# Performance work log

Measured on AMD Instinct MI355X. Metric: run time of the kernel, lower is better.

Reference implementation:

```python
import jax, jax.numpy as jnp
import numpy as np

BATCH = 32
LATENT = 128
NODE_DIM = 8
MAX_NODES = 512
H_NODE = 128   # node_generator hidden
H_EDGE = 64    # edge_generator hidden


def setup_inputs() -> dict:
    key = jax.random.key(0)
    ks = jax.random.split(key, 9)
    s = 0.02
    return {
        "z":   jax.random.normal(ks[0], (BATCH, LATENT), dtype=jnp.float32),
        "W1":  jax.random.normal(ks[1], (LATENT, H_NODE), dtype=jnp.float32) * s,
        "b1":  jnp.zeros((H_NODE,), dtype=jnp.float32),
        "W2":  jax.random.normal(ks[2], (H_NODE, MAX_NODES * NODE_DIM), dtype=jnp.float32) * s,
        "b2":  jnp.zeros((MAX_NODES * NODE_DIM,), dtype=jnp.float32),
        "E1":  jax.random.normal(ks[3], (2 * NODE_DIM, H_EDGE), dtype=jnp.float32) * s,
        "eb1": jnp.zeros((H_EDGE,), dtype=jnp.float32),
        "E2":  jax.random.normal(ks[4], (H_EDGE, 1), dtype=jnp.float32) * s,
        "eb2": jnp.zeros((1,), dtype=jnp.float32),
    }


def reference(z, W1, b1, W2, b2, E1, eb1, E2, eb2):
    B = z.shape[0]
    # node generator: Linear -> ReLU -> Linear, view to [B, N, node_dim]
    h = jax.nn.relu(z @ W1 + b1)
    nodes = (h @ W2 + b2).reshape(B, MAX_NODES, NODE_DIM)

    # all unordered pairs i < j (static indices)
    iu, ju = np.triu_indices(MAX_NODES, k=1)  # [P]
    pair = jnp.concatenate([nodes[:, iu, :], nodes[:, ju, :]], axis=-1)  # [B, P, 2d]

    # edge generator: Linear -> ReLU -> Linear -> Sigmoid
    he = jax.nn.relu(jnp.einsum("bpd,dh->bph", pair, E1) + eb1)
    p = jax.nn.sigmoid(jnp.einsum("bph,ho->bpo", he, E2) + eb2)[..., 0]  # [B, P]

    adj = jnp.zeros((B, MAX_NODES, MAX_NODES), dtype=p.dtype)
    adj = adj.at[:, iu, ju].set(p).at[:, ju, iu].set(p)
    return nodes, adj
```

## Files before the change

### kernel.cpp

```cpp
#include <hip/hip_runtime.h>

#define BATCH 32
#define LATENT 128
#define NODE_DIM 8
#define MAX_NODES 512
#define H_NODE 128
#define H_EDGE 64

typedef _Float16 h2 __attribute__((ext_vector_type(2)));

static __device__ __forceinline__ h2 u32_to_h2(unsigned int x) {
    union { unsigned int u; h2 h; } c; c.u = x; return c.h;
}
static __device__ __forceinline__ unsigned int h2_to_u32(h2 x) {
    union { unsigned int u; h2 h; } c; c.h = x; return c.u;
}

#if __has_builtin(__builtin_amdgcn_fdot2)
#define FDOT2(a, b, c) __builtin_amdgcn_fdot2((a), (b), (c), false)
#else
#define FDOT2(a, b, c) ((c) + (float)(a).x * (float)(b).x + (float)(a).y * (float)(b).y)
#endif

#define UPKH_DWORDS (BATCH * 32 * MAX_NODES)
#define VH_DWORDS   (BATCH * MAX_NODES * 32)

__global__ __launch_bounds__(128) void h_gen(
    const float* __restrict__ z, const float* __restrict__ W1,
    const float* __restrict__ b1, float* __restrict__ Hws)
{
    const int b = blockIdx.x, tid = threadIdx.x;
    __shared__ float sz[LATENT];
    sz[tid] = z[b * LATENT + tid];
    __syncthreads();
    float acc = b1[tid];
#pragma unroll 8
    for (int k = 0; k < LATENT; ++k)
        acc += sz[k] * W1[k * H_NODE + tid];
    Hws[b * H_NODE + tid] = fmaxf(acc, 0.0f);
}

__global__ __launch_bounds__(256) void gen_nodes_uv(
    const float* __restrict__ Hws, const float* __restrict__ W2,
    const float* __restrict__ b2,  const float* __restrict__ E1,
    const float* __restrict__ eb1, const float* __restrict__ E2,
    float* __restrict__ nodes_out, unsigned int* __restrict__ UPKH,
    unsigned int* __restrict__ VH, unsigned int* __restrict__ E2H)
{
    const int b      = blockIdx.x;
    const int mslice = blockIdx.y;
    const int tid    = threadIdx.x;
    const int i0     = mslice * 32;

    __shared__ float sh[H_NODE];
    __shared__ float sE1[2 * NODE_DIM][H_EDGE];
    __shared__ float sEb1[H_EDGE];
    __shared__ float sN[32][NODE_DIM];

    if (tid < H_NODE) sh[tid] = Hws[b * H_NODE + tid];
    for (int idx = tid; idx < 2 * NODE_DIM * H_EDGE; idx += 256)
        (&sE1[0][0])[idx] = E1[idx];
    if (tid < H_EDGE) sEb1[tid] = eb1[tid];

    if (b == 0 && mslice == 0 && tid < 32) {
        h2 w = { (_Float16)E2[2 * tid], (_Float16)E2[2 * tid + 1] };
        E2H[tid] = h2_to_u32(w);
    }
    __syncthreads();

    const int m = mslice * 256 + tid;
    float acc = b2[m];
#pragma unroll 8
    for (int k = 0; k < H_NODE; ++k)
        acc += sh[k] * W2[(size_t)k * (MAX_NODES * NODE_DIM) + m];
    nodes_out[(size_t)b * (MAX_NODES * NODE_DIM) + m] = acc;
    sN[tid >> 3][tid & 7] = acc;
    __syncthreads();

    {
        const int il = tid & 31;
        const int cg = tid >> 5;
#pragma unroll
        for (int rep = 0; rep < 4; ++rep) {
            const int c2 = rep * 8 + cg;
            const int c  = 2 * c2;
            float ua = sEb1[c], ub = sEb1[c + 1];
#pragma unroll
            for (int d = 0; d < NODE_DIM; ++d) {
                const float nd = sN[il][d];
                ua += nd * sE1[d][c];
                ub += nd * sE1[d][c + 1];
            }
            h2 uu = { (_Float16)ua, (_Float16)ub };
            UPKH[((size_t)b * 32 + c2) * MAX_NODES + i0 + il] = h2_to_u32(uu);
        }
    }
    {
        const int jl = tid >> 3;
        const int cq = tid & 7;
#pragma unroll
        for (int rep = 0; rep < 4; ++rep) {
            const int c2 = rep * 8 + cq;
            const int c  = 2 * c2;
            float va = 0.f, vb = 0.f;
#pragma unroll
            for (int d = 0; d < NODE_DIM; ++d) {
                const float nd = sN[jl][d];
                va += nd * sE1[NODE_DIM + d][c];
                vb += nd * sE1[NODE_DIM + d][c + 1];
            }
            h2 vv = { (_Float16)va, (_Float16)vb };
            VH[((size_t)(b * MAX_NODES + i0 + jl) << 5) + c2] = h2_to_u32(vv);
        }
    }
}

__global__ __launch_bounds__(256, 4) void edge_gen(
    const unsigned int* __restrict__ UPKH, const unsigned int* __restrict__ VH,
    const unsigned int* __restrict__ E2H, const float* __restrict__ eb2,
    float* __restrict__ adj)
{
    const int b = blockIdx.y;
    int t = blockIdx.x, bi = 0;
    while (t >= 16 - 2 * bi) { t -= 16 - 2 * bi; ++bi; }
    const int jt = 2 * bi + t;
    const bool partial = (jt >> 1) == bi;

    const int tid  = threadIdx.x;
    const int lane = tid & 63;
    const int wv   = tid >> 6;
    const int i0 = bi * 64, j0 = jt * 32;
    const int i  = i0 + lane;

    __shared__ unsigned int sV[32 * 32];
    __shared__ float P[32][65];

    {
        const float4* src = (const float4*)(VH + ((size_t)(b * MAX_NODES + j0) << 5));
        ((float4*)sV)[tid] = src[tid];
    }

    unsigned int uA[32];
#pragma unroll
    for (int c2 = 0; c2 < 32; ++c2)
        uA[c2] = UPKH[((size_t)b * 32 + c2) * MAX_NODES + i];

    unsigned int wb[32];
#pragma unroll
    for (int c2 = 0; c2 < 32; ++c2) wb[c2] = E2H[c2];

    const float bias = eb2[0];
    float* adjb = adj + (size_t)b * MAX_NODES * MAX_NODES;
    const h2 zh = { (_Float16)0.f, (_Float16)0.f };
    __syncthreads();

#pragma unroll 1
    for (int jj = 0; jj < 8; ++jj) {
        const int jl = wv * 8 + jj;
        const int j  = j0 + jl;
        const float4* vrow = (const float4*)&sV[jl * 32];

        float a0 = 0.f, a1 = 0.f;
#pragma unroll
        for (int q = 0; q < 8; ++q) {
            union { float4 f4; unsigned int u[4]; } vv;
            vv.f4 = vrow[q];
#pragma unroll
            for (int k = 0; k < 4; ++k) {
                const int c2 = 4 * q + k;
                const h2 v = u32_to_h2(vv.u[k]);
                const h2 w = u32_to_h2(wb[c2]);
                h2 s = u32_to_h2(uA[c2]) + v;
                s = __builtin_elementwise_max(s, zh);
                if (k & 1) a1 = FDOT2(s, w, a1);
                else       a0 = FDOT2(s, w, a0);
            }
        }
        const float x = a0 + a1 + bias;
        const float p = __builtin_amdgcn_rcpf(1.0f + __expf(-x));

        if (!partial) {
            adjb[(size_t)j * MAX_NODES + i] = p;
            P[jl][lane] = p;
        } else {
            if (i < j)       { adjb[(size_t)j * MAX_NODES + i] = p;
                               adjb[(size_t)i * MAX_NODES + j] = p; }
            else if (i == j)   adjb[(size_t)j * MAX_NODES + i] = 0.0f;
        }
    }

    if (!partial) {
        __syncthreads();
        const int r = tid & 63;
        const int q = tid >> 6;
        const size_t rowbase = (size_t)(i0 + r) * MAX_NODES + j0 + q * 8;
        float4 o0, o1;
        o0.x = P[q * 8 + 0][r]; o0.y = P[q * 8 + 1][r];
        o0.z = P[q * 8 + 2][r]; o0.w = P[q * 8 + 3][r];
        o1.x = P[q * 8 + 4][r]; o1.y = P[q * 8 + 5][r];
        o1.z = P[q * 8 + 6][r]; o1.w = P[q * 8 + 7][r];
        *(float4*)&adjb[rowbase]     = o0;
        *(float4*)&adjb[rowbase + 4] = o1;
    }
}

extern "C" void kernel_launch(void* const* d_in, const int* in_sizes, int n_in,
                              void* d_out, int out_size, void* d_ws, size_t ws_size,
                              hipStream_t stream)
{
    const float* z   = (const float*)d_in[0];
    const float* W1  = (const float*)d_in[1];
    const float* b1  = (const float*)d_in[2];
    const float* W2  = (const float*)d_in[3];
    const float* b2  = (const float*)d_in[4];
    const float* E1  = (const float*)d_in[5];
    const float* eb1 = (const float*)d_in[6];
    const float* E2  = (const float*)d_in[7];
    const float* eb2 = (const float*)d_in[8];

    float* nodes_out = (float*)d_out;
    float* adj       = (float*)d_out + BATCH * MAX_NODES * NODE_DIM;

    unsigned int* UPKH = (unsigned int*)d_ws;
    unsigned int* VHp  = UPKH + UPKH_DWORDS;
    unsigned int* E2H  = VHp + VH_DWORDS;
    float*        Hws  = (float*)(E2H + 32);

    h_gen<<<BATCH, 128, 0, stream>>>(z, W1, b1, Hws);

    dim3 g1(BATCH, 16);
    gen_nodes_uv<<<g1, 256, 0, stream>>>(Hws, W2, b2, E1, eb1, E2,
                                         nodes_out, UPKH, VHp, E2H);

    dim3 g2(72, BATCH);
    edge_gen<<<g2, 256, 0, stream>>>(UPKH, VHp, E2H, eb2, adj);
}
```

Before: 46.29 us.

## Halve edge tile width to 16 columns and fully unroll four-column ILP

The edge kernel now covers 64x16 tiles instead of 64x32, so the grid doubles to 144 blocks per batch. Each wave handles four j columns at once with a fully unrolled loop and eight independent accumulators, replacing the serial 8-iteration loop. The aim is more blocks to fill the GPU and more instruction-level parallelism per thread. In exchange, the per-thread UPKH row loads and E2H loads are repeated across twice as many blocks, and register pressure rises.

```diff
diff --git a/kernel.cpp b/kernel.cpp
--- a/kernel.cpp
+++ b/kernel.cpp
@@ -122,22 +122,22 @@
 {
     const int b = blockIdx.y;
     int t = blockIdx.x, bi = 0;
-    while (t >= 16 - 2 * bi) { t -= 16 - 2 * bi; ++bi; }
-    const int jt = 2 * bi + t;
-    const bool partial = (jt >> 1) == bi;
+    while (t >= 32 - 4 * bi) { t -= 32 - 4 * bi; ++bi; }
+    const int jt = 4 * bi + t;
+    const bool partial = (jt >> 2) == bi;
 
     const int tid  = threadIdx.x;
     const int lane = tid & 63;
     const int wv   = tid >> 6;
-    const int i0 = bi * 64, j0 = jt * 32;
+    const int i0 = bi * 64, j0 = jt * 16;
     const int i  = i0 + lane;
 
-    __shared__ unsigned int sV[32 * 32];
-    __shared__ float P[32][65];
-
-    {
-        const float4* src = (const float4*)(VH + ((size_t)(b * MAX_NODES + j0) << 5));
-        ((float4*)sV)[tid] = src[tid];
+    __shared__ unsigned int sV[16 * 32];
+    __shared__ float P[16][65];
+
+    if (tid < 128) {
+        const uint4* src = (const uint4*)(VH + ((size_t)(b * MAX_NODES + j0) << 5));
+        ((uint4*)sV)[tid] = src[tid];
     }
 
     unsigned int uA[32];
@@ -154,31 +154,56 @@
     const h2 zh = { (_Float16)0.f, (_Float16)0.f };
     __syncthreads();
 
-#pragma unroll 1
-    for (int jj = 0; jj < 8; ++jj) {
-        const int jl = wv * 8 + jj;
+    const int jbase = wv * 4;
+    const uint4* vr0 = (const uint4*)&sV[(jbase + 0) * 32];
+    const uint4* vr1 = (const uint4*)&sV[(jbase + 1) * 32];
+    const uint4* vr2 = (const uint4*)&sV[(jbase + 2) * 32];
+    const uint4* vr3 = (const uint4*)&sV[(jbase + 3) * 32];
+
+    float acc0a = 0.f, acc0b = 0.f, acc1a = 0.f, acc1b = 0.f;
+    float acc2a = 0.f, acc2b = 0.f, acc3a = 0.f, acc3b = 0.f;
+
+#pragma unroll
+    for (int q = 0; q < 8; ++q) {
+        union { uint4 u4; unsigned int u[4]; } v0, v1, v2, v3;
+        v0.u4 = vr0[q]; v1.u4 = vr1[q]; v2.u4 = vr2[q]; v3.u4 = vr3[q];
+#pragma unroll
+        for (int k = 0; k < 4; ++k) {
+            const int c2 = 4 * q + k;
+            const h2 u = u32_to_h2(uA[c2]);
+            const h2 w = u32_to_h2(wb[c2]);
+            h2 s0 = u + u32_to_h2(v0.u[k]);
+            h2 s1 = u + u32_to_h2(v1.u[k]);
+            h2 s2 = u + u32_to_h2(v2.u[k]);
+            h2 s3 = u + u32_to_h2(v3.u[k]);
+            s0 = __builtin_elementwise_max(s0, zh);
+            s1 = __builtin_elementwise_max(s1, zh);
+            s2 = __builtin_elementwise_max(s2, zh);
+            s3 = __builtin_elementwise_max(s3, zh);
+            if (k & 1) {
+                acc0b = FDOT2(s0, w, acc0b); acc1b = FDOT2(s1, w, acc1b);
+                acc2b = FDOT2(s2, w, acc2b); acc3b = FDOT2(s3, w, acc3b);
+            } else {
+                acc0a = FDOT2(s0, w, acc0a); acc1a = FDOT2(s1, w, acc1a);
+                acc2a = FDOT2(s2, w, acc2a); acc3a = FDOT2(s3, w, acc3a);
+            }
+        }
+    }
+
+    float px[4];
+    px[0] = acc0a + acc0b + bias;
+    px[1] = acc1a + acc1b + bias;
+    px[2] = acc2a + acc2b + bias;
+    px[3] = acc3a + acc3b + bias;
+#pragma unroll
+    for (int jj = 0; jj < 4; ++jj)
+        px[jj] = __builtin_amdgcn_rcpf(1.0f + __expf(-px[jj]));
+
+#pragma unroll
+    for (int jj = 0; jj < 4; ++jj) {
+        const int jl = jbase + jj;
         const int j  = j0 + jl;
-        const float4* vrow = (const float4*)&sV[jl * 32];
-
-        float a0 = 0.f, a1 = 0.f;
-#pragma unroll
-        for (int q = 0; q < 8; ++q) {
-            union { float4 f4; unsigned int u[4]; } vv;
-            vv.f4 = vrow[q];
-#pragma unroll
-            for (int k = 0; k < 4; ++k) {
-                const int c2 = 4 * q + k;
-                const h2 v = u32_to_h2(vv.u[k]);
-                const h2 w = u32_to_h2(wb[c2]);
-                h2 s = u32_to_h2(uA[c2]) + v;
-                s = __builtin_elementwise_max(s, zh);
-                if (k & 1) a1 = FDOT2(s, w, a1);
-                else       a0 = FDOT2(s, w, a0);
-            }
-        }
-        const float x = a0 + a1 + bias;
-        const float p = __builtin_amdgcn_rcpf(1.0f + __expf(-x));
-
+        const float p = px[jj];
         if (!partial) {
             adjb[(size_t)j * MAX_NODES + i] = p;
             P[jl][lane] = p;
@@ -193,14 +218,10 @@
         __syncthreads();
         const int r = tid & 63;
         const int q = tid >> 6;
-        const size_t rowbase = (size_t)(i0 + r) * MAX_NODES + j0 + q * 8;
-        float4 o0, o1;
-        o0.x = P[q * 8 + 0][r]; o0.y = P[q * 8 + 1][r];
-        o0.z = P[q * 8 + 2][r]; o0.w = P[q * 8 + 3][r];
-        o1.x = P[q * 8 + 4][r]; o1.y = P[q * 8 + 5][r];
-        o1.z = P[q * 8 + 6][r]; o1.w = P[q * 8 + 7][r];
-        *(float4*)&adjb[rowbase]     = o0;
-        *(float4*)&adjb[rowbase + 4] = o1;
+        float4 o;
+        o.x = P[q * 4 + 0][r]; o.y = P[q * 4 + 1][r];
+        o.z = P[q * 4 + 2][r]; o.w = P[q * 4 + 3][r];
+        *(float4*)&adjb[(size_t)(i0 + r) * MAX_NODES + j0 + q * 4] = o;
     }
 }
 
@@ -232,6 +253,6 @@
     gen_nodes_uv<<<g1, 256, 0, stream>>>(Hws, W2, b2, E1, eb1, E2,
                                          nodes_out, UPKH, VHp, E2H);
 
-    dim3 g2(72, BATCH);
+    dim3 g2(144, BATCH);
     edge_gen<<<g2, 256, 0, stream>>>(UPKH, VHp, E2H, eb2, adj);
 }
```

Result: slower. 66.69 us (+44.1%).

## Handle diagonal edge tiles as full 64x64 blocks with LDS-transposed symmetric stores

Applied to the files above, without the earlier changes.

Diagonal tiles used to be two 64x32 partial blocks that wrote scattered strided stores in both orientations. They are now one 64x64 block per diagonal that computes all 64 columns into shared memory, then writes the symmetric tile with coalesced float4 row stores and zeros the diagonal. This cuts the grid from 72 to 64 blocks per batch and removes the uncoalesced scalar writes. In exchange the diagonal blocks compute redundant pairs (j<i) and the larger shared memory footprint may lower occupancy.

```diff
diff --git a/kernel.cpp b/kernel.cpp
--- a/kernel.cpp
+++ b/kernel.cpp
@@ -115,29 +115,58 @@
     }
 }
 
+static __device__ __forceinline__ float edge_dot(
+    const uint4* vrow, const unsigned int (&uA)[32], const unsigned int (&wb)[32])
+{
+    const h2 zh = { (_Float16)0.f, (_Float16)0.f };
+    float a0 = 0.f, a1 = 0.f;
+#pragma unroll
+    for (int q = 0; q < 8; ++q) {
+        union { uint4 u4; unsigned int u[4]; } vv;
+        vv.u4 = vrow[q];
+#pragma unroll
+        for (int k = 0; k < 4; ++k) {
+            const int c2 = 4 * q + k;
+            const h2 v = u32_to_h2(vv.u[k]);
+            const h2 w = u32_to_h2(wb[c2]);
+            h2 s = u32_to_h2(uA[c2]) + v;
+            s = __builtin_elementwise_max(s, zh);
+            if (k & 1) a1 = FDOT2(s, w, a1);
+            else       a0 = FDOT2(s, w, a0);
+        }
+    }
+    return a0 + a1;
+}
+
 __global__ __launch_bounds__(256, 4) void edge_gen(
     const unsigned int* __restrict__ UPKH, const unsigned int* __restrict__ VH,
     const unsigned int* __restrict__ E2H, const float* __restrict__ eb2,
     float* __restrict__ adj)
 {
     const int b = blockIdx.y;
-    int t = blockIdx.x, bi = 0;
-    while (t >= 16 - 2 * bi) { t -= 16 - 2 * bi; ++bi; }
-    const int jt = 2 * bi + t;
-    const bool partial = (jt >> 1) == bi;
-
+    const int x = blockIdx.x;
     const int tid  = threadIdx.x;
     const int lane = tid & 63;
     const int wv   = tid >> 6;
-    const int i0 = bi * 64, j0 = jt * 32;
+
+    __shared__ unsigned int sV[64 * 32];
+    __shared__ float P[64][65];
+
+    int bi, j0, nj;
+    if (x < 8) { bi = x; j0 = bi * 64; nj = 64; }
+    else {
+        int k = x - 8; bi = 0;
+        while (k >= 14 - 2 * bi) { k -= 14 - 2 * bi; ++bi; }
+        j0 = (2 * bi + 2 + k) * 32; nj = 32;
+    }
+    const int i0 = bi * 64;
     const int i  = i0 + lane;
 
-    __shared__ unsigned int sV[32 * 32];
-    __shared__ float P[32][65];
-
     {
-        const float4* src = (const float4*)(VH + ((size_t)(b * MAX_NODES + j0) << 5));
-        ((float4*)sV)[tid] = src[tid];
+        const uint4* src = (const uint4*)(VH + ((size_t)(b * MAX_NODES + j0) << 5));
+        uint4* dst = (uint4*)sV;
+        dst[tid] = src[tid];
+        if (nj == 64) dst[tid + 256] = src[tid + 256];
     }
 
     unsigned int uA[32];
@@ -151,45 +180,18 @@
 
     const float bias = eb2[0];
     float* adjb = adj + (size_t)b * MAX_NODES * MAX_NODES;
-    const h2 zh = { (_Float16)0.f, (_Float16)0.f };
-    __syncthreads();
-
+    __syncthreads();
+
+    if (nj == 32) {
 #pragma unroll 1
-    for (int jj = 0; jj < 8; ++jj) {
-        const int jl = wv * 8 + jj;
-        const int j  = j0 + jl;
-        const float4* vrow = (const float4*)&sV[jl * 32];
-
-        float a0 = 0.f, a1 = 0.f;
-#pragma unroll
-        for (int q = 0; q < 8; ++q) {
-            union { float4 f4; unsigned int u[4]; } vv;
-            vv.f4 = vrow[q];
-#pragma unroll
-            for (int k = 0; k < 4; ++k) {
-                const int c2 = 4 * q + k;
-                const h2 v = u32_to_h2(vv.u[k]);
-                const h2 w = u32_to_h2(wb[c2]);
-                h2 s = u32_to_h2(uA[c2]) + v;
-                s = __builtin_elementwise_max(s, zh);
-                if (k & 1) a1 = FDOT2(s, w, a1);
-                else       a0 = FDOT2(s, w, a0);
-            }
-        }
-        const float x = a0 + a1 + bias;
-        const float p = __builtin_amdgcn_rcpf(1.0f + __expf(-x));
-
-        if (!partial) {
+        for (int jj = 0; jj < 8; ++jj) {
+            const int jl = wv * 8 + jj;
+            const int j  = j0 + jl;
+            const float xs = edge_dot((const uint4*)&sV[jl * 32], uA, wb) + bias;
+            const float p  = __builtin_amdgcn_rcpf(1.0f + __expf(-xs));
             adjb[(size_t)j * MAX_NODES + i] = p;
             P[jl][lane] = p;
-        } else {
-            if (i < j)       { adjb[(size_t)j * MAX_NODES + i] = p;
-                               adjb[(size_t)i * MAX_NODES + j] = p; }
-            else if (i == j)   adjb[(size_t)j * MAX_NODES + i] = 0.0f;
-        }
-    }
-
-    if (!partial) {
+        }
         __syncthreads();
         const int r = tid & 63;
         const int q = tid >> 6;
@@ -201,6 +203,38 @@
         o1.z = P[q * 8 + 6][r]; o1.w = P[q * 8 + 7][r];
         *(float4*)&adjb[rowbase]     = o0;
         *(float4*)&adjb[rowbase + 4] = o1;
+    } else {
+#pragma unroll 1
+        for (int jj = 0; jj < 16; ++jj) {
+            const int jl = wv * 16 + jj;
+            const float xs = edge_dot((const uint4*)&sV[jl * 32], uA, wb) + bias;
+            P[jl][lane] = __builtin_amdgcn_rcpf(1.0f + __expf(-xs));
+        }
+        __syncthreads();
+        const int r = tid & 63;
+        const int q = tid >> 6;
+#pragma unroll
+        for (int g = 0; g < 4; ++g) {
+            const int cb = q * 16 + g * 4;
+            float4 o;
+            {
+                const int c = cb + 0;
+                o.x = (r < c) ? P[c][r] : ((r > c) ? P[r][c] : 0.0f);
+            }
+            {
+                const int c = cb + 1;
+                o.y = (r < c) ? P[c][r] : ((r > c) ? P[r][c] : 0.0f);
+            }
+            {
+                const int c = cb + 2;
+                o.z = (r < c) ? P[c][r] : ((r > c) ? P[r][c] : 0.0f);
+            }
+            {
+                const int c = cb + 3;
+                o.w = (r < c) ? P[c][r] : ((r > c) ? P[r][c] : 0.0f);
+            }
+            *(float4*)&adjb[(size_t)(i0 + r) * MAX_NODES + i0 + cb] = o;
+        }
     }
 }
 
@@ -232,6 +266,6 @@
     gen_nodes_uv<<<g1, 256, 0, stream>>>(Hws, W2, b2, E1, eb1, E2,
                                          nodes_out, UPKH, VHp, E2H);
 
-    dim3 g2(72, BATCH);
+    dim3 g2(64, BATCH);
     edge_gen<<<g2, 256, 0, stream>>>(UPKH, VHp, E2H, eb2, adj);
 }
```

New measurement: 53.95 us. +16.6%, slower.

## Use 128x32 off-diagonal tiles in edge_gen with two rows per thread

Applied to the files above, without the earlier changes.

Reworks edge_gen block mapping so most off-diagonal tiles cover 128 i-rows by 32 j-columns, with each thread computing two i values and reusing each shared V row for both. Diagonal regions keep the 64x32 partial and full paths, and the grid drops from 72 to 48 blocks per batch. This is meant to halve LDS V reads and per-block setup per output. It raises register pressure and reduces block count, which may hurt occupancy.

```diff
diff --git a/kernel.cpp b/kernel.cpp
--- a/kernel.cpp
+++ b/kernel.cpp
@@ -115,35 +115,60 @@
     }
 }
 
+static __device__ __forceinline__ float edge_dot(
+    const uint4* vrow, const unsigned int (&uA)[32], const unsigned int (&wb)[32])
+{
+    const h2 zh = { (_Float16)0.f, (_Float16)0.f };
+    float a0 = 0.f, a1 = 0.f;
+#pragma unroll
+    for (int q = 0; q < 8; ++q) {
+        union { uint4 u4; unsigned int u[4]; } vv;
+        vv.u4 = vrow[q];
+#pragma unroll
+        for (int k = 0; k < 4; ++k) {
+            const int c2 = 4 * q + k;
+            h2 s = u32_to_h2(uA[c2]) + u32_to_h2(vv.u[k]);
+            s = __builtin_elementwise_max(s, zh);
+            if (k & 1) a1 = FDOT2(s, u32_to_h2(wb[c2]), a1);
+            else       a0 = FDOT2(s, u32_to_h2(wb[c2]), a0);
+        }
+    }
+    return a0 + a1;
+}
+
 __global__ __launch_bounds__(256, 4) void edge_gen(
     const unsigned int* __restrict__ UPKH, const unsigned int* __restrict__ VH,
     const unsigned int* __restrict__ E2H, const float* __restrict__ eb2,
     float* __restrict__ adj)
 {
     const int b = blockIdx.y;
-    int t = blockIdx.x, bi = 0;
-    while (t >= 16 - 2 * bi) { t -= 16 - 2 * bi; ++bi; }
-    const int jt = 2 * bi + t;
-    const bool partial = (jt >> 1) == bi;
-
+    const int x = blockIdx.x;
     const int tid  = threadIdx.x;
     const int lane = tid & 63;
     const int wv   = tid >> 6;
-    const int i0 = bi * 64, j0 = jt * 32;
-    const int i  = i0 + lane;
 
     __shared__ unsigned int sV[32 * 32];
-    __shared__ float P[32][65];
+    __shared__ float P[32][129];
+
+    int i0, j0, type;
+    if (x < 24) {
+        int bb, jt;
+        if (x < 12)      { bb = 0; jt = 4 + x; }
+        else if (x < 20) { bb = 1; jt = 8 + (x - 12); }
+        else             { bb = 2; jt = 12 + (x - 20); }
+        i0 = bb * 128; j0 = jt * 32; type = 0;
+    } else if (x < 32) {
+        const int idx = x - 24, a = idx >> 1, hf = idx & 1;
+        i0 = a * 128; j0 = a * 128 + 64 + hf * 32; type = 1;
+    } else {
+        const int idx = x - 32, bi = idx >> 1;
+        i0 = bi * 64; j0 = bi * 64 + (idx & 1) * 32; type = 2;
+    }
 
     {
-        const float4* src = (const float4*)(VH + ((size_t)(b * MAX_NODES + j0) << 5));
-        ((float4*)sV)[tid] = src[tid];
-    }
-
-    unsigned int uA[32];
-#pragma unroll
-    for (int c2 = 0; c2 < 32; ++c2)
-        uA[c2] = UPKH[((size_t)b * 32 + c2) * MAX_NODES + i];
+        const uint4* src = (const uint4*)(VH + ((size_t)(b * MAX_NODES + j0) << 5));
+        ((uint4*)sV)[tid] = src[tid];
+    }
 
     unsigned int wb[32];
 #pragma unroll
@@ -152,55 +177,105 @@
     const float bias = eb2[0];
     float* adjb = adj + (size_t)b * MAX_NODES * MAX_NODES;
     const h2 zh = { (_Float16)0.f, (_Float16)0.f };
-    __syncthreads();
+
+    if (type == 0) {
+        const int iA = i0 + lane, iB = iA + 64;
+        unsigned int uA[32], uB[32];
+#pragma unroll
+        for (int c2 = 0; c2 < 32; ++c2) {
+            const unsigned int* base = &UPKH[((size_t)b * 32 + c2) * MAX_NODES];
+            uA[c2] = base[iA];
+            uB[c2] = base[iB];
+        }
+        __syncthreads();
 
 #pragma unroll 1
-    for (int jj = 0; jj < 8; ++jj) {
-        const int jl = wv * 8 + jj;
-        const int j  = j0 + jl;
-        const float4* vrow = (const float4*)&sV[jl * 32];
-
-        float a0 = 0.f, a1 = 0.f;
-#pragma unroll
-        for (int q = 0; q < 8; ++q) {
-            union { float4 f4; unsigned int u[4]; } vv;
-            vv.f4 = vrow[q];
-#pragma unroll
-            for (int k = 0; k < 4; ++k) {
-                const int c2 = 4 * q + k;
-                const h2 v = u32_to_h2(vv.u[k]);
-                const h2 w = u32_to_h2(wb[c2]);
-                h2 s = u32_to_h2(uA[c2]) + v;
-                s = __builtin_elementwise_max(s, zh);
-                if (k & 1) a1 = FDOT2(s, w, a1);
-                else       a0 = FDOT2(s, w, a0);
+        for (int jj = 0; jj < 8; ++jj) {
+            const int jl = wv * 8 + jj;
+            const int j  = j0 + jl;
+            const uint4* vrow = (const uint4*)&sV[jl * 32];
+
+            float aA0 = 0.f, aA1 = 0.f, aB0 = 0.f, aB1 = 0.f;
+#pragma unroll
+            for (int q = 0; q < 8; ++q) {
+                union { uint4 u4; unsigned int u[4]; } vv;
+                vv.u4 = vrow[q];
+#pragma unroll
+                for (int k = 0; k < 4; ++k) {
+                    const int c2 = 4 * q + k;
+                    const h2 v = u32_to_h2(vv.u[k]);
+                    const h2 w = u32_to_h2(wb[c2]);
+                    h2 sA = u32_to_h2(uA[c2]) + v;
+                    h2 sB = u32_to_h2(uB[c2]) + v;
+                    sA = __builtin_elementwise_max(sA, zh);
+                    sB = __builtin_elementwise_max(sB, zh);
+                    if (k & 1) { aA1 = FDOT2(sA, w, aA1); aB1 = FDOT2(sB, w, aB1); }
+                    else       { aA0 = FDOT2(sA, w, aA0); aB0 = FDOT2(sB, w, aB0); }
+                }
             }
-        }
-        const float x = a0 + a1 + bias;
-        const float p = __builtin_amdgcn_rcpf(1.0f + __expf(-x));
+            const float xA = aA0 + aA1 + bias;
+            const float xB = aB0 + aB1 + bias;
+            const float pA = __builtin_amdgcn_rcpf(1.0f + __expf(-xA));
+            const float pB = __builtin_amdgcn_rcpf(1.0f + __expf(-xB));
+
+            adjb[(size_t)j * MAX_NODES + iA] = pA;
+            adjb[(size_t)j * MAX_NODES + iB] = pB;
+            P[jl][lane]      = pA;
+            P[jl][64 + lane] = pB;
+        }
+        __syncthreads();
+
+        const int r = tid & 127;
+        const int h = tid >> 7;
+        const size_t rowbase = (size_t)(i0 + r) * MAX_NODES + j0 + h * 16;
+#pragma unroll
+        for (int g = 0; g < 4; ++g) {
+            const int c0 = h * 16 + 4 * g;
+            float4 o;
+            o.x = P[c0 + 0][r]; o.y = P[c0 + 1][r];
+            o.z = P[c0 + 2][r]; o.w = P[c0 + 3][r];
+            *(float4*)&adjb[rowbase + 4 * g] = o;
+        }
+    } else {
+        const int i = i0 + lane;
+        unsigned int uA[32];
+#pragma unroll
+        for (int c2 = 0; c2 < 32; ++c2)
+            uA[c2] = UPKH[((size_t)b * 32 + c2) * MAX_NODES + i];
+        __syncthreads();
+
+        const bool partial = (type == 2);
+
+#pragma unroll 1
+        for (int jj = 0; jj < 8; ++jj) {
+            const int jl = wv * 8 + jj;
+            const int j  = j0 + jl;
+            const float xs = edge_dot((const uint4*)&sV[jl * 32], uA, wb) + bias;
+            const float p  = __builtin_amdgcn_rcpf(1.0f + __expf(-xs));
+
+            if (!partial) {
+                adjb[(size_t)j * MAX_NODES + i] = p;
+                P[jl][lane] = p;
+            } else {
+                if (i < j)       { adjb[(size_t)j * MAX_NODES + i] = p;
+                                   adjb[(size_t)i * MAX_NODES + j] = p; }
+                else if (i == j)   adjb[(size_t)j * MAX_NODES + i] = 0.0f;
+            }
+        }
 
         if (!partial) {
-            adjb[(size_t)j * MAX_NODES + i] = p;
-            P[jl][lane] = p;
-        } else {
-            if (i < j)       { adjb[(size_t)j * MAX_NODES + i] = p;
-                               adjb[(size_t)i * MAX_NODES + j] = p; }
-            else if (i == j)   adjb[(size_t)j * MAX_NODES + i] = 0.0f;
-        }
-    }
-
-    if (!partial) {
-        __syncthreads();
-        const int r = tid & 63;
-        const int q = tid >> 6;
-        const size_t rowbase = (size_t)(i0 + r) * MAX_NODES + j0 + q * 8;
-        float4 o0, o1;
-        o0.x = P[q * 8 + 0][r]; o0.y = P[q * 8 + 1][r];
-        o0.z = P[q * 8 + 2][r]; o0.w = P[q * 8 + 3][r];
-        o1.x = P[q * 8 + 4][r]; o1.y = P[q * 8 + 5][r];
-        o1.z = P[q * 8 + 6][r]; o1.w = P[q * 8 + 7][r];
-        *(float4*)&adjb[rowbase]     = o0;
-        *(float4*)&adjb[rowbase + 4] = o1;
+            __syncthreads();
+            const int r = tid & 63;
+            const int q = tid >> 6;
+            const size_t rowbase = (size_t)(i0 + r) * MAX_NODES + j0 + q * 8;
+            float4 o0, o1;
+            o0.x = P[q * 8 + 0][r]; o0.y = P[q * 8 + 1][r];
+            o0.z = P[q * 8 + 2][r]; o0.w = P[q * 8 + 3][r];
+            o1.x = P[q * 8 + 4][r]; o1.y = P[q * 8 + 5][r];
+            o1.z = P[q * 8 + 6][r]; o1.w = P[q * 8 + 7][r];
+            *(float4*)&adjb[rowbase]     = o0;
+            *(float4*)&adjb[rowbase + 4] = o1;
+        }
     }
 }
 
@@ -232,6 +307,6 @@
     gen_nodes_uv<<<g1, 256, 0, stream>>>(Hws, W2, b2, E1, eb1, E2,
                                          nodes_out, UPKH, VHp, E2H);
 
-    dim3 g2(72, BATCH);
+    dim3 g2(48, BATCH);
     edge_gen<<<g2, 256, 0, stream>>>(UPKH, VHp, E2H, eb2, adj);
 }
```

New measurement: 49.07 us. 6.0% more time.
